# Performance work log

Measured on AMD Instinct MI355X. Metric: run time of the kernel, lower is better.

Reference implementation:

```python
import jax, jax.numpy as jnp
import numpy as np

N, E = 20000, 320000
IN_C, HID, OUT_C, HEADS = 512, 32, 40, 8
NEG_SLOPE = 0.2


def setup_inputs() -> dict:
    key = jax.random.key(0)
    ks = jax.random.split(key, 10)
    x = jax.random.normal(ks[0], (N, IN_C), dtype=jnp.float32)
    edge_index = jax.random.randint(ks[1], (2, E), 0, N, dtype=jnp.int64)
    s1 = 1.0 / np.sqrt(IN_C)
    s2 = 1.0 / np.sqrt(HEADS * HID)
    return {
        "x": x,
        "edge_index": edge_index,
        "w1": jax.random.normal(ks[2], (IN_C, HEADS * HID), dtype=jnp.float32) * s1,
        "att_src1": jax.random.normal(ks[3], (HEADS, HID), dtype=jnp.float32) * s2,
        "att_dst1": jax.random.normal(ks[4], (HEADS, HID), dtype=jnp.float32) * s2,
        "b1": jnp.zeros((HEADS * HID,), dtype=jnp.float32),
        "w2": jax.random.normal(ks[5], (HEADS * HID, OUT_C), dtype=jnp.float32) * s2,
        "att_src2": jax.random.normal(ks[6], (1, OUT_C), dtype=jnp.float32) * 0.15,
        "att_dst2": jax.random.normal(ks[7], (1, OUT_C), dtype=jnp.float32) * 0.15,
        "b2": jnp.zeros((OUT_C,), dtype=jnp.float32),
    }


def gat_conv(x, src, dst, w, att_src, att_dst, bias, heads, out_c, concat):
    n = x.shape[0]
    h = (x @ w).reshape(n, heads, out_c)            # [N,H,C]
    a_s = jnp.sum(h * att_src, axis=-1)             # [N,H]
    a_d = jnp.sum(h * att_dst, axis=-1)             # [N,H]
    e = jax.nn.leaky_relu(a_s[src] + a_d[dst], NEG_SLOPE)  # [E,H]
    # segment softmax over destination nodes (self-loops guarantee nonempty)
    m = jax.ops.segment_max(e, dst, num_segments=n)
    e = jnp.exp(e - m[dst])
    z = jax.ops.segment_sum(e, dst, num_segments=n)
    alpha = e / (z[dst] + 1e-16)                    # [E,H]
    msg = alpha[:, :, None] * h[src]                # [E,H,C]
    out = jax.ops.segment_sum(msg, dst, num_segments=n)  # [N,H,C]
    out = out.reshape(n, heads * out_c) if concat else out.mean(axis=1)
    return out + bias


def reference(x, edge_index, w1, att_src1, att_dst1, b1, w2, att_src2, att_dst2, b2):
    n = x.shape[0]
    loops = jnp.arange(n, dtype=edge_index.dtype)
    src = jnp.concatenate([edge_index[0], loops])
    dst = jnp.concatenate([edge_index[1], loops])
    h = gat_conv(x, src, dst, w1, att_src1, att_dst1, b1, HEADS, HID, True)
    h = jax.nn.elu(h)
    out = gat_conv(h, src, dst, w2, att_src2, att_dst2, b2, 1, OUT_C, False)
    return jax.nn.log_softmax(out, axis=1)
```

## Files before the change

### kernel.cpp

```cpp
#include <hip/hip_runtime.h>
#include <hip/hip_bf16.h>
#include <math.h>

#define N_NODES 20000
#define N_EDGES 320000
#define ET (N_EDGES + N_NODES)
#define IN_C 512
#define HEADS 8
#define HID 32
#define HH (HEADS * HID)
#define OUT_C 40
#define NEG_SLOPE 0.2f

typedef __attribute__((ext_vector_type(8))) short short8;
typedef __attribute__((ext_vector_type(4))) float floatx4;

static __device__ __forceinline__ unsigned short f2bf(float f) {
  __hip_bfloat16 h = __float2bfloat16(f);
  return *(unsigned short*)&h;
}
static __device__ __forceinline__ float bf2f_lo(unsigned int u) {
  return __uint_as_float(u << 16);
}
static __device__ __forceinline__ float bf2f_hi(unsigned int u) {
  return __uint_as_float(u & 0xFFFF0000u);
}

#define WCONV_BLOCKS (IN_C * HH / 256)
#define W2CONV_BLOCKS (HH * OUT_C / 256)
#define COUNT_BLOCKS ((ET + 255) / 256)
__global__ __launch_bounds__(256) void prep_kernel(
    const float* __restrict__ w1, const float* __restrict__ w2,
    const int* __restrict__ ei, unsigned short* __restrict__ wbT,
    unsigned short* __restrict__ w2bT, int* __restrict__ deg) {
  if (blockIdx.x < WCONV_BLOCKS) {
    int j = blockIdx.x * 256 + threadIdx.x;
    int k = j >> 8, n = j & 255;
    wbT[(size_t)n * IN_C + k] = f2bf(w1[j]);
  } else if (blockIdx.x < WCONV_BLOCKS + W2CONV_BLOCKS) {
    int j = (blockIdx.x - WCONV_BLOCKS) * 256 + threadIdx.x;
    int k = j / OUT_C, oc = j % OUT_C;
    w2bT[oc * HH + k] = f2bf(w2[j]);
  } else {
    int e = (blockIdx.x - WCONV_BLOCKS - W2CONV_BLOCKS) * 256 + threadIdx.x;
    if (e < ET) {
      int dst = (e < N_EDGES) ? ei[N_EDGES + e] : (e - N_EDGES);
      atomicAdd(&deg[dst], 1);
    }
  }
}

#define BM 64
#define BN 128
#define BK 32
#define APAD 40
#define GY ((N_NODES + BM - 1) / BM)
#define GEMM_BLOCKS (2 * GY)
__global__ __launch_bounds__(256) void gemm1_kernel(
    const float* __restrict__ X, const unsigned short* __restrict__ BT,
    const float* __restrict__ bias, const float* __restrict__ asrc,
    const float* __restrict__ adst, unsigned short* __restrict__ C,
    float* __restrict__ as1, float* __restrict__ ad1,
    const int* __restrict__ deg, int* __restrict__ offs, int* __restrict__ cursor) {
  if (blockIdx.x >= GEMM_BLOCKS) {
    __shared__ int wsum[4];
    int t = threadIdx.x;
    int4 buf[20];
    int s = 0;
    if (t < 250) {
      const int4* dp = (const int4*)deg + t * 20;
#pragma unroll
      for (int i = 0; i < 20; i++) {
        buf[i] = dp[i];
        s += buf[i].x + buf[i].y + buf[i].z + buf[i].w;
      }
    }
    int lane = t & 63, w = t >> 6;
    int inc = s;
    for (int o = 1; o < 64; o <<= 1) {
      int u = __shfl_up(inc, o, 64);
      if (lane >= o) inc += u;
    }
    if (lane == 63) wsum[w] = inc;
    __syncthreads();
    int waveOff = 0;
    for (int i = 0; i < w; i++) waveOff += wsum[i];
    int running = waveOff + inc - s;
    if (t < 250) {
      int base = t * 80;
#pragma unroll
      for (int i = 0; i < 20; i++) {
        int4 v = buf[i];
        int4 o;
        o.x = running;
        o.y = o.x + v.x;
        o.z = o.y + v.y;
        o.w = o.z + v.z;
        running = o.w + v.w;
        *(int4*)(offs + base + i * 4) = o;
        *(int4*)(cursor + base + i * 4) = o;
      }
    }
    if (t == 0) offs[N_NODES] = ET;
    return;
  }
  int d = blockIdx.x;
  int by, bx;
  const int FULL = (GY / 8) * 16;
  if (d < FULL) {
    int c = d >> 4, j = d & 15;
    by = c * 8 + (j & 7);
    bx = j >> 3;
  } else {
    int dd = d - FULL;
    by = (GY / 8) * 8 + (dd & 0);
    bx = dd;
  }
  __shared__ unsigned short As[BM][APAD];
  __shared__ unsigned short Bs[BN][APAD];
  const int tid = threadIdx.x;
  const int lane = tid & 63, wave = tid >> 6;
  const int wm = (wave & 1) * 32;
  const int wn = (wave >> 1) * 64;
  const int r16 = lane & 15, q = lane >> 4;
  const int rowBase = by * BM;
  const int colBase = bx * BN;
  floatx4 acc[2][4] = {};

  for (int k0 = 0; k0 < IN_C; k0 += BK) {
    {
      int row = tid >> 2, kc = (tid & 3) * 8;
      int arow = rowBase + row;
      float4 v0 = make_float4(0.f, 0.f, 0.f, 0.f), v1 = v0;
      if (arow < N_NODES) {
        const float* p = X + (size_t)arow * IN_C + k0 + kc;
        v0 = *(const float4*)p;
        v1 = *(const float4*)(p + 4);
      }
      unsigned short tmp[8] = {f2bf(v0.x), f2bf(v0.y), f2bf(v0.z), f2bf(v0.w),
                               f2bf(v1.x), f2bf(v1.y), f2bf(v1.z), f2bf(v1.w)};
      *(float4*)&As[row][kc] = *(const float4*)tmp;
    }
#pragma unroll
    for (int i = 0; i < 2; i++) {
      int c = tid + i * 256;
      int row = c >> 2, kc = (c & 3) * 8;
      float4 v = *(const float4*)(BT + (size_t)(colBase + row) * IN_C + k0 + kc);
      *(float4*)&Bs[row][kc] = v;
    }
    __syncthreads();
    short8 afrag[2], bfrag[4];
#pragma unroll
    for (int mt = 0; mt < 2; mt++)
      afrag[mt] = *(const short8*)&As[wm + mt * 16 + r16][q * 8];
#pragma unroll
    for (int nt = 0; nt < 4; nt++)
      bfrag[nt] = *(const short8*)&Bs[wn + nt * 16 + r16][q * 8];
#pragma unroll
    for (int mt = 0; mt < 2; mt++)
#pragma unroll
      for (int nt = 0; nt < 4; nt++)
        acc[mt][nt] = __builtin_amdgcn_mfma_f32_16x16x32_bf16(
            afrag[mt], bfrag[nt], acc[mt][nt], 0, 0, 0);
    __syncthreads();
  }
  float sa[4], sd[4], bbv[4];
#pragma unroll
  for (int nt = 0; nt < 4; nt++) {
    int col = colBase + wn + nt * 16 + r16;
    sa[nt] = asrc[col];
    sd[nt] = adst[col];
    bbv[nt] = bias[col];
  }
  const int headBase = (colBase + wn) >> 5;
#pragma unroll
  for (int mt = 0; mt < 2; mt++) {
#pragma unroll
    for (int nt = 0; nt < 4; nt++) {
      int col = colBase + wn + nt * 16 + r16;
#pragma unroll
      for (int r = 0; r < 4; r++) {
        int row = rowBase + wm + mt * 16 + q * 4 + r;
        if (row < N_NODES) C[(size_t)row * HH + col] = f2bf(acc[mt][nt][r] + bbv[nt]);
      }
    }
#pragma unroll
    for (int h = 0; h < 2; h++) {
#pragma unroll
      for (int r = 0; r < 4; r++) {
        float v0 = acc[mt][2 * h][r] + bbv[2 * h];
        float v1 = acc[mt][2 * h + 1][r] + bbv[2 * h + 1];
        float ps = v0 * sa[2 * h] + v1 * sa[2 * h + 1];
        float pd = v0 * sd[2 * h] + v1 * sd[2 * h + 1];
#pragma unroll
        for (int o = 1; o < 16; o <<= 1) {
          ps += __shfl_xor(ps, o, 64);
          pd += __shfl_xor(pd, o, 64);
        }
        if (r16 == 0) {
          int row = rowBase + wm + mt * 16 + q * 4 + r;
          if (row < N_NODES) {
            as1[row * HEADS + headBase + h] = ps;
            ad1[row * HEADS + headBase + h] = pd;
          }
        }
      }
    }
  }
}

#define FILL_BLOCKS ((ET + 255) / 256)
__global__ __launch_bounds__(256) void fill_kernel(
    const int* __restrict__ ei, int* __restrict__ cursor, int* __restrict__ csr) {
  int e = blockIdx.x * 256 + threadIdx.x;
  if (e >= ET) return;
  int src, dst;
  if (e < N_EDGES) { src = ei[e]; dst = ei[N_EDGES + e]; }
  else { src = e - N_EDGES; dst = src; }
  int pos = atomicAdd(&cursor[dst], 1);
  csr[pos] = src;
}

#define NPB 16
#define H2ROW 264
__global__ __launch_bounds__(512, 8) void layer1_fused_kernel(
    const unsigned short* __restrict__ h1b, const float* __restrict__ as1,
    const float* __restrict__ ad1, const int* __restrict__ offs,
    const int* __restrict__ csr, const float* __restrict__ b1,
    const unsigned short* __restrict__ w2bT, const float* __restrict__ b2,
    const float* __restrict__ asrc2, const float* __restrict__ adst2,
    float* __restrict__ h3, float* __restrict__ as2, float* __restrict__ ad2) {
  __shared__ __align__(16) unsigned short h2s[NPB][H2ROW];
  __shared__ float psum[3][NPB], pdsum[3][NPB];
  const int tid = threadIdx.x;
  const int wave = tid >> 6, lane = tid & 63;
  const int r16 = lane & 15, q = lane >> 4;
  const int nodeBase = blockIdx.x * NPB;

  const int strm = lane >> 5;
  const int l32 = lane & 31;
  const int c8 = l32 * 8;
  const int head = l32 >> 2;
  float4 bb = *(const float4*)(b1 + c8 + strm * 4);
#pragma unroll
  for (int i = 0; i < 2; i++) {
    int local = wave * 2 + i;
    int n = nodeBase + local;
    int beg = offs[n], end = offs[n + 1];
    int cnt = end - beg;
    float ad = ad1[n * HEADS + head];
    float acc[8] = {};
    float l = 0.f;
    for (int kb = 0; kb < cnt; kb += 64) {
      int nb = (cnt - kb < 64) ? (cnt - kb) : 64;
      int myidx = (lane < nb) ? csr[beg + kb + lane] : 0;
      int j = strm;
      if (j < nb) {
        int src = __shfl(myidx, j, 64);
        uint4 r = *(const uint4*)(h1b + ((unsigned)src << 8) + c8);
        float e = as1[src * HEADS + head];
        for (j += 2; j < nb; j += 2) {
          int src2 = __shfl(myidx, j, 64);
          uint4 r2 = *(const uint4*)(h1b + ((unsigned)src2 << 8) + c8);
          float e2 = as1[src2 * HEADS + head];
          float tt = e + ad;
          tt = (tt > 0.f) ? tt : NEG_SLOPE * tt;
          float p = __expf(tt);
          l += p;
          acc[0] = fmaf(p, bf2f_lo(r.x), acc[0]);
          acc[1] = fmaf(p, bf2f_hi(r.x), acc[1]);
          acc[2] = fmaf(p, bf2f_lo(r.y), acc[2]);
          acc[3] = fmaf(p, bf2f_hi(r.y), acc[3]);
          acc[4] = fmaf(p, bf2f_lo(r.z), acc[4]);
          acc[5] = fmaf(p, bf2f_hi(r.z), acc[5]);
          acc[6] = fmaf(p, bf2f_lo(r.w), acc[6]);
          acc[7] = fmaf(p, bf2f_hi(r.w), acc[7]);
          r = r2; e = e2;
        }
        float tt = e + ad;
        tt = (tt > 0.f) ? tt : NEG_SLOPE * tt;
        float p = __expf(tt);
        l += p;
        acc[0] = fmaf(p, bf2f_lo(r.x), acc[0]);
        acc[1] = fmaf(p, bf2f_hi(r.x), acc[1]);
        acc[2] = fmaf(p, bf2f_lo(r.y), acc[2]);
        acc[3] = fmaf(p, bf2f_hi(r.y), acc[3]);
        acc[4] = fmaf(p, bf2f_lo(r.z), acc[4]);
        acc[5] = fmaf(p, bf2f_hi(r.z), acc[5]);
        acc[6] = fmaf(p, bf2f_lo(r.w), acc[6]);
        acc[7] = fmaf(p, bf2f_hi(r.w), acc[7]);
      }
    }
#pragma unroll
    for (int j = 0; j < 8; j++) acc[j] += __shfl_xor(acc[j], 32, 64);
    l += __shfl_xor(l, 32, 64);
    float li = 1.f / (l + 1e-16f);
    float v0 = (strm ? acc[4] : acc[0]) * li + bb.x;
    float v1 = (strm ? acc[5] : acc[1]) * li + bb.y;
    float v2 = (strm ? acc[6] : acc[2]) * li + bb.z;
    float v3 = (strm ? acc[7] : acc[3]) * li + bb.w;
    v0 = (v0 > 0.f) ? v0 : __expf(v0) - 1.f;
    v1 = (v1 > 0.f) ? v1 : __expf(v1) - 1.f;
    v2 = (v2 > 0.f) ? v2 : __expf(v2) - 1.f;
    v3 = (v3 > 0.f) ? v3 : __expf(v3) - 1.f;
    uint2 w;
    w.x = (unsigned)f2bf(v0) | ((unsigned)f2bf(v1) << 16);
    w.y = (unsigned)f2bf(v2) | ((unsigned)f2bf(v3) << 16);
    *(uint2*)&h2s[local][c8 + strm * 4] = w;
  }
  __syncthreads();

  if (wave < 3) {
    int col = wave * 16 + r16;
    int colc = (col < OUT_C) ? col : 0;
    short8 bfrag[8];
#pragma unroll
    for (int s = 0; s < 8; s++)
      bfrag[s] = *(const short8*)(w2bT + colc * HH + s * 32 + q * 8);
    float sa = 0.f, sd = 0.f, b2c = 0.f;
    if (col < OUT_C) { sa = asrc2[col]; sd = adst2[col]; b2c = b2[col]; }
    floatx4 dacc = {};
#pragma unroll
    for (int s = 0; s < 8; s++) {
      short8 afrag = *(const short8*)&h2s[r16][s * 32 + q * 8];
      dacc = __builtin_amdgcn_mfma_f32_16x16x32_bf16(afrag, bfrag[s], dacc, 0, 0, 0);
    }
    float psr[4], pdr[4];
#pragma unroll
    for (int r = 0; r < 4; r++) {
      float val = dacc[r] + b2c;
      if (col < OUT_C)
        h3[(size_t)(nodeBase + q * 4 + r) * OUT_C + col] = val;
      psr[r] = val * sa;
      pdr[r] = val * sd;
    }
#pragma unroll
    for (int o = 8; o > 0; o >>= 1) {
#pragma unroll
      for (int r = 0; r < 4; r++) {
        psr[r] += __shfl_down(psr[r], o, 16);
        pdr[r] += __shfl_down(pdr[r], o, 16);
      }
    }
    if (r16 == 0) {
#pragma unroll
      for (int r = 0; r < 4; r++) {
        psum[wave][q * 4 + r] = psr[r];
        pdsum[wave][q * 4 + r] = pdr[r];
      }
    }
  }
  __syncthreads();
  if (tid < NPB) {
    as2[nodeBase + tid] = psum[0][tid] + psum[1][tid] + psum[2][tid];
    ad2[nodeBase + tid] = pdsum[0][tid] + pdsum[1][tid] + pdsum[2][tid];
  }
}

__global__ __launch_bounds__(256) void agg2_kernel(
    const float* __restrict__ h3, const float* __restrict__ as2,
    const float* __restrict__ ad2, const int* __restrict__ offs,
    const int* __restrict__ csr, const float* __restrict__ b2,
    float* __restrict__ out) {
  int n = blockIdx.x * 4 + (threadIdx.x >> 6);
  int t = threadIdx.x & 63;
  bool act = (t < OUT_C);
  int beg = offs[n], end = offs[n + 1];
  int cnt = end - beg;
  float ad = ad2[n];
  float l = 0.f;
  float a0 = 0.f, a1 = 0.f, a2 = 0.f, a3 = 0.f;
  for (int kb = 0; kb < cnt; kb += 64) {
    int nb = (cnt - kb < 64) ? (cnt - kb) : 64;
    int sj = 0;
    float pj = 0.f;
    if (t < nb) {
      sj = csr[beg + kb + t];
      float e = as2[sj] + ad;
      e = (e > 0.f) ? e : NEG_SLOPE * e;
      pj = __expf(e);
    }
    float ll = pj;
#pragma unroll
    for (int o = 32; o > 0; o >>= 1) ll += __shfl_xor(ll, o, 64);
    l += ll;
    int j = 0;
    for (; j + 3 < nb; j += 4) {
      int s0 = __shfl(sj, j, 64), s1 = __shfl(sj, j + 1, 64);
      int s2 = __shfl(sj, j + 2, 64), s3 = __shfl(sj, j + 3, 64);
      float p0 = __shfl(pj, j, 64), p1 = __shfl(pj, j + 1, 64);
      float p2 = __shfl(pj, j + 2, 64), p3 = __shfl(pj, j + 3, 64);
      float h0 = act ? h3[(size_t)s0 * OUT_C + t] : 0.f;
      float h1 = act ? h3[(size_t)s1 * OUT_C + t] : 0.f;
      float h2 = act ? h3[(size_t)s2 * OUT_C + t] : 0.f;
      float h3v = act ? h3[(size_t)s3 * OUT_C + t] : 0.f;
      a0 = fmaf(p0, h0, a0);
      a1 = fmaf(p1, h1, a1);
      a2 = fmaf(p2, h2, a2);
      a3 = fmaf(p3, h3v, a3);
    }
    for (; j < nb; j++) {
      int s0 = __shfl(sj, j, 64);
      float p0 = __shfl(pj, j, 64);
      float h0 = act ? h3[(size_t)s0 * OUT_C + t] : 0.f;
      a0 = fmaf(p0, h0, a0);
    }
  }
  float acc = (a0 + a1) + (a2 + a3);
  float v = acc / (l + 1e-16f) + (act ? b2[t] : 0.f);
  float x = act ? v : -INFINITY;
  float mx = x;
  for (int o = 32; o > 0; o >>= 1) mx = fmaxf(mx, __shfl_down(mx, o, 64));
  mx = __shfl(mx, 0, 64);
  float ex = act ? __expf(v - mx) : 0.f;
  float s = ex;
  for (int o = 32; o > 0; o >>= 1) s += __shfl_down(s, o, 64);
  s = __shfl(s, 0, 64);
  if (act) out[(size_t)n * OUT_C + t] = v - mx - logf(s);
}

extern "C" void kernel_launch(void* const* d_in, const int* in_sizes, int n_in,
                              void* d_out, int out_size, void* d_ws, size_t ws_size,
                              hipStream_t stream) {
  const float* x     = (const float*)d_in[0];
  const int*   ei    = (const int*)d_in[1];
  const float* w1    = (const float*)d_in[2];
  const float* asrc1 = (const float*)d_in[3];
  const float* adst1 = (const float*)d_in[4];
  const float* b1    = (const float*)d_in[5];
  const float* w2    = (const float*)d_in[6];
  const float* asrc2 = (const float*)d_in[7];
  const float* adst2 = (const float*)d_in[8];
  const float* b2    = (const float*)d_in[9];
  float* out = (float*)d_out;

  float* fw = (float*)d_ws;
  float* as1   = fw;  fw += (size_t)N_NODES * HEADS;
  float* ad1   = fw;  fw += (size_t)N_NODES * HEADS;
  float* h3    = fw;  fw += (size_t)N_NODES * OUT_C;
  float* as2   = fw;  fw += N_NODES;
  float* ad2   = fw;  fw += N_NODES;
  unsigned short* h1b  = (unsigned short*)fw;  fw += (size_t)N_NODES * HH / 2;
  unsigned short* wbT  = (unsigned short*)fw;  fw += (size_t)IN_C * HH / 2;
  unsigned short* w2bT = (unsigned short*)fw;  fw += (size_t)HH * OUT_C / 2;
  int* deg    = (int*)fw;
  int* offs   = deg + N_NODES;
  int* cursor = offs + N_NODES + 4;
  int* csr    = cursor + N_NODES;

  hipMemsetAsync(deg, 0, N_NODES * sizeof(int), stream);

  prep_kernel<<<WCONV_BLOCKS + W2CONV_BLOCKS + COUNT_BLOCKS, 256, 0, stream>>>(
      w1, w2, ei, wbT, w2bT, deg);
  gemm1_kernel<<<GEMM_BLOCKS + 1, 256, 0, stream>>>(
      x, wbT, b1, asrc1, adst1, h1b, as1, ad1, deg, offs, cursor);
  fill_kernel<<<FILL_BLOCKS, 256, 0, stream>>>(ei, cursor, csr);
  layer1_fused_kernel<<<N_NODES / NPB, 512, 0, stream>>>(
      h1b, as1, ad1, offs, csr, b1, w2bT, b2, asrc2, adst2, h3, as2, ad2);
  agg2_kernel<<<N_NODES / 4, 256, 0, stream>>>(h3, as2, ad2, offs, csr, b2, out);
}
```

Measured before the change: 204.9 us.

## Widen GEMM tile to full output width and deepen gather prefetch pipeline

The first-layer GEMM now covers all 256 output columns per block (BN 128→256), so each block reads and converts its X tile from fp32 once instead of twice, and the block-swizzle mapping is removed. Each wave now holds 4x4 accumulator tiles, which raises register pressure and halves the block count. The layer-1 aggregation loop now prefetches two neighbor rows ahead instead of one, and the bias load moves after the loop. Occupancy in the launch bounds drops from 8 to 7 to make room for the extra registers.

New measurement: 205.6 us. Within noise of the previous version (+0.4%).

```diff
diff --git a/kernel.cpp b/kernel.cpp
--- a/kernel.cpp
+++ b/kernel.cpp
@@ -51,18 +51,17 @@
 }
 
 #define BM 64
-#define BN 128
+#define BN 256
 #define BK 32
 #define APAD 40
 #define GY ((N_NODES + BM - 1) / BM)
-#define GEMM_BLOCKS (2 * GY)
 __global__ __launch_bounds__(256) void gemm1_kernel(
     const float* __restrict__ X, const unsigned short* __restrict__ BT,
     const float* __restrict__ bias, const float* __restrict__ asrc,
     const float* __restrict__ adst, unsigned short* __restrict__ C,
     float* __restrict__ as1, float* __restrict__ ad1,
     const int* __restrict__ deg, int* __restrict__ offs, int* __restrict__ cursor) {
-  if (blockIdx.x >= GEMM_BLOCKS) {
+  if (blockIdx.x >= GY) {
     __shared__ int wsum[4];
     int t = threadIdx.x;
     int4 buf[20];
@@ -104,28 +103,14 @@
     if (t == 0) offs[N_NODES] = ET;
     return;
   }
-  int d = blockIdx.x;
-  int by, bx;
-  const int FULL = (GY / 8) * 16;
-  if (d < FULL) {
-    int c = d >> 4, j = d & 15;
-    by = c * 8 + (j & 7);
-    bx = j >> 3;
-  } else {
-    int dd = d - FULL;
-    by = (GY / 8) * 8 + (dd & 0);
-    bx = dd;
-  }
   __shared__ unsigned short As[BM][APAD];
   __shared__ unsigned short Bs[BN][APAD];
   const int tid = threadIdx.x;
   const int lane = tid & 63, wave = tid >> 6;
-  const int wm = (wave & 1) * 32;
-  const int wn = (wave >> 1) * 64;
+  const int wn = wave * 64;
   const int r16 = lane & 15, q = lane >> 4;
-  const int rowBase = by * BM;
-  const int colBase = bx * BN;
-  floatx4 acc[2][4] = {};
+  const int rowBase = blockIdx.x * BM;
+  floatx4 acc[4][4] = {};
 
   for (int k0 = 0; k0 < IN_C; k0 += BK) {
     {
@@ -142,22 +127,22 @@
       *(float4*)&As[row][kc] = *(const float4*)tmp;
     }
 #pragma unroll
-    for (int i = 0; i < 2; i++) {
+    for (int i = 0; i < 4; i++) {
       int c = tid + i * 256;
       int row = c >> 2, kc = (c & 3) * 8;
-      float4 v = *(const float4*)(BT + (size_t)(colBase + row) * IN_C + k0 + kc);
+      float4 v = *(const float4*)(BT + (size_t)row * IN_C + k0 + kc);
       *(float4*)&Bs[row][kc] = v;
     }
     __syncthreads();
-    short8 afrag[2], bfrag[4];
-#pragma unroll
-    for (int mt = 0; mt < 2; mt++)
-      afrag[mt] = *(const short8*)&As[wm + mt * 16 + r16][q * 8];
+    short8 afrag[4], bfrag[4];
+#pragma unroll
+    for (int mt = 0; mt < 4; mt++)
+      afrag[mt] = *(const short8*)&As[mt * 16 + r16][q * 8];
 #pragma unroll
     for (int nt = 0; nt < 4; nt++)
       bfrag[nt] = *(const short8*)&Bs[wn + nt * 16 + r16][q * 8];
 #pragma unroll
-    for (int mt = 0; mt < 2; mt++)
+    for (int mt = 0; mt < 4; mt++)
 #pragma unroll
       for (int nt = 0; nt < 4; nt++)
         acc[mt][nt] = __builtin_amdgcn_mfma_f32_16x16x32_bf16(
@@ -167,20 +152,20 @@
   float sa[4], sd[4], bbv[4];
 #pragma unroll
   for (int nt = 0; nt < 4; nt++) {
-    int col = colBase + wn + nt * 16 + r16;
+    int col = wn + nt * 16 + r16;
     sa[nt] = asrc[col];
     sd[nt] = adst[col];
     bbv[nt] = bias[col];
   }
-  const int headBase = (colBase + wn) >> 5;
-#pragma unroll
-  for (int mt = 0; mt < 2; mt++) {
+  const int headBase = wn >> 5;
+#pragma unroll
+  for (int mt = 0; mt < 4; mt++) {
 #pragma unroll
     for (int nt = 0; nt < 4; nt++) {
-      int col = colBase + wn + nt * 16 + r16;
+      int col = wn + nt * 16 + r16;
 #pragma unroll
       for (int r = 0; r < 4; r++) {
-        int row = rowBase + wm + mt * 16 + q * 4 + r;
+        int row = rowBase + mt * 16 + q * 4 + r;
         if (row < N_NODES) C[(size_t)row * HH + col] = f2bf(acc[mt][nt][r] + bbv[nt]);
       }
     }
@@ -198,7 +183,7 @@
           pd += __shfl_xor(pd, o, 64);
         }
         if (r16 == 0) {
-          int row = rowBase + wm + mt * 16 + q * 4 + r;
+          int row = rowBase + mt * 16 + q * 4 + r;
           if (row < N_NODES) {
             as1[row * HEADS + headBase + h] = ps;
             ad1[row * HEADS + headBase + h] = pd;
@@ -223,7 +208,22 @@
 
 #define NPB 16
 #define H2ROW 264
-__global__ __launch_bounds__(512, 8) void layer1_fused_kernel(
+#define CONSUME(rr, ee)                              \
+  do {                                               \
+    float tt = (ee) + ad;                            \
+    tt = (tt > 0.f) ? tt : NEG_SLOPE * tt;           \
+    float p = __expf(tt);                            \
+    l += p;                                          \
+    acc[0] = fmaf(p, bf2f_lo((rr).x), acc[0]);       \
+    acc[1] = fmaf(p, bf2f_hi((rr).x), acc[1]);       \
+    acc[2] = fmaf(p, bf2f_lo((rr).y), acc[2]);       \
+    acc[3] = fmaf(p, bf2f_hi((rr).y), acc[3]);       \
+    acc[4] = fmaf(p, bf2f_lo((rr).z), acc[4]);       \
+    acc[5] = fmaf(p, bf2f_hi((rr).z), acc[5]);       \
+    acc[6] = fmaf(p, bf2f_lo((rr).w), acc[6]);       \
+    acc[7] = fmaf(p, bf2f_hi((rr).w), acc[7]);       \
+  } while (0)
+__global__ __launch_bounds__(512, 7) void layer1_fused_kernel(
     const unsigned short* __restrict__ h1b, const float* __restrict__ as1,
     const float* __restrict__ ad1, const int* __restrict__ offs,
     const int* __restrict__ csr, const float* __restrict__ b1,
@@ -241,7 +241,6 @@
   const int l32 = lane & 31;
   const int c8 = l32 * 8;
   const int head = l32 >> 2;
-  float4 bb = *(const float4*)(b1 + c8 + strm * 4);
 #pragma unroll
   for (int i = 0; i < 2; i++) {
     int local = wave * 2 + i;
@@ -256,45 +255,36 @@
       int myidx = (lane < nb) ? csr[beg + kb + lane] : 0;
       int j = strm;
       if (j < nb) {
-        int src = __shfl(myidx, j, 64);
-        uint4 r = *(const uint4*)(h1b + ((unsigned)src << 8) + c8);
-        float e = as1[src * HEADS + head];
-        for (j += 2; j < nb; j += 2) {
-          int src2 = __shfl(myidx, j, 64);
-          uint4 r2 = *(const uint4*)(h1b + ((unsigned)src2 << 8) + c8);
-          float e2 = as1[src2 * HEADS + head];
-          float tt = e + ad;
-          tt = (tt > 0.f) ? tt : NEG_SLOPE * tt;
-          float p = __expf(tt);
-          l += p;
-          acc[0] = fmaf(p, bf2f_lo(r.x), acc[0]);
-          acc[1] = fmaf(p, bf2f_hi(r.x), acc[1]);
-          acc[2] = fmaf(p, bf2f_lo(r.y), acc[2]);
-          acc[3] = fmaf(p, bf2f_hi(r.y), acc[3]);
-          acc[4] = fmaf(p, bf2f_lo(r.z), acc[4]);
-          acc[5] = fmaf(p, bf2f_hi(r.z), acc[5]);
-          acc[6] = fmaf(p, bf2f_lo(r.w), acc[6]);
-          acc[7] = fmaf(p, bf2f_hi(r.w), acc[7]);
-          r = r2; e = e2;
+        int s0 = __shfl(myidx, j, 64);
+        uint4 r0 = *(const uint4*)(h1b + ((unsigned)s0 << 8) + c8);
+        float e0 = as1[s0 * HEADS + head];
+        uint4 r1{};
+        float e1 = 0.f;
+        bool have1 = (j + 2 < nb);
+        if (have1) {
+          int s1 = __shfl(myidx, j + 2, 64);
+          r1 = *(const uint4*)(h1b + ((unsigned)s1 << 8) + c8);
+          e1 = as1[s1 * HEADS + head];
         }
-        float tt = e + ad;
-        tt = (tt > 0.f) ? tt : NEG_SLOPE * tt;
-        float p = __expf(tt);
-        l += p;
-        acc[0] = fmaf(p, bf2f_lo(r.x), acc[0]);
-        acc[1] = fmaf(p, bf2f_hi(r.x), acc[1]);
-        acc[2] = fmaf(p, bf2f_lo(r.y), acc[2]);
-        acc[3] = fmaf(p, bf2f_hi(r.y), acc[3]);
-        acc[4] = fmaf(p, bf2f_lo(r.z), acc[4]);
-        acc[5] = fmaf(p, bf2f_hi(r.z), acc[5]);
-        acc[6] = fmaf(p, bf2f_lo(r.w), acc[6]);
-        acc[7] = fmaf(p, bf2f_hi(r.w), acc[7]);
+        for (int j2 = j + 4; j2 < nb; j2 += 2) {
+          int s2 = __shfl(myidx, j2, 64);
+          uint4 r2 = *(const uint4*)(h1b + ((unsigned)s2 << 8) + c8);
+          float e2 = as1[s2 * HEADS + head];
+          CONSUME(r0, e0);
+          r0 = r1; e0 = e1; r1 = r2; e1 = e2;
+        }
+        if (have1) {
+          CONSUME(r0, e0);
+          r0 = r1; e0 = e1;
+        }
+        CONSUME(r0, e0);
       }
     }
 #pragma unroll
     for (int j = 0; j < 8; j++) acc[j] += __shfl_xor(acc[j], 32, 64);
     l += __shfl_xor(l, 32, 64);
     float li = 1.f / (l + 1e-16f);
+    float4 bb = *(const float4*)(b1 + c8 + strm * 4);
     float v0 = (strm ? acc[4] : acc[0]) * li + bb.x;
     float v1 = (strm ? acc[5] : acc[1]) * li + bb.y;
     float v2 = (strm ? acc[6] : acc[2]) * li + bb.z;
@@ -452,7 +442,7 @@
 
   prep_kernel<<<WCONV_BLOCKS + W2CONV_BLOCKS + COUNT_BLOCKS, 256, 0, stream>>>(
       w1, w2, ei, wbT, w2bT, deg);
-  gemm1_kernel<<<GEMM_BLOCKS + 1, 256, 0, stream>>>(
+  gemm1_kernel<<<GY + 1, 256, 0, stream>>>(
       x, wbT, b1, asrc1, adst1, h1b, as1, ad1, deg, offs, cursor);
   fill_kernel<<<FILL_BLOCKS, 256, 0, stream>>>(ei, cursor, csr);
   layer1_fused_kernel<<<N_NODES / NPB, 512, 0, stream>>>(
```
